# Performance work log

Hardware: AMD Instinct MI355X
Metric: run time of the kernel (lower is better)

Reference implementation:

```python
import jax, jax.numpy as jnp
import numpy as np

COS_BASIS_NO = 13
COS_SHIFT = 1.0
COS_SCALE = 3.0


def make_cos_basis(T_no):
    # [13, T_no] raised-cosine basis in log-time, matching the torch loop
    i = jnp.arange(COS_BASIS_NO, dtype=jnp.float32)[:, None]
    phi = 0.5 * jnp.pi * i
    x = jnp.arange(T_no, dtype=jnp.float32)[None, :]
    raw = COS_SCALE * jnp.log(x + COS_SHIFT)
    basis = 0.5 * jnp.cos(raw - phi) + 0.5
    mask = (raw >= phi - jnp.pi) & (raw <= phi + jnp.pi)
    return jnp.where(mask, basis, jnp.float32(0.0))


def causal_conv(x, kern):
    # x: [T, S], kern: [S, K] (unflipped, kern[:,0] = weight on x[t-1]).
    # Matches torch: pad K zeros in front, depthwise conv with flipped kernel, drop last.
    T, S = x.shape
    K = kern.shape[1]
    xp = jnp.pad(x, ((K, 0), (0, 0)))            # [T+K, S]
    lhs = xp.T[None]                              # [1, S, T+K]
    rhs = kern[:, None, ::-1]                     # [S, 1, K]
    out = jax.lax.conv_general_dilated(
        lhs, rhs, window_strides=(1,), padding='VALID',
        dimension_numbers=('NCW', 'OIW', 'NCW'), feature_group_count=S)
    return out[0].T[:-1]                          # [T, S]


def setup_inputs() -> dict:
    T_data, T_no, sub_no, E_no, I_no = 500000, 200, 20, 200, 50
    key = jax.random.key(0)
    ks = jax.random.split(key, 8)
    S_e = (jax.random.uniform(ks[0], (T_data, E_no)) < 0.05).astype(jnp.float32)
    S_i = (jax.random.uniform(ks[1], (T_data, I_no)) < 0.05).astype(jnp.float32)
    Z = (jax.random.uniform(ks[2], (T_data, sub_no)) < 0.10).astype(jnp.float32)
    C_syn_e = jax.nn.one_hot(jax.random.randint(ks[3], (E_no,), 0, sub_no), sub_no).T.astype(jnp.float32)
    C_syn_i = jax.nn.one_hot(jax.random.randint(ks[4], (I_no,), 0, sub_no), sub_no).T.astype(jnp.float32)
    C_den = (jax.random.uniform(ks[5], (sub_no, sub_no)) < 0.1).astype(jnp.float32)
    Tau_syn = jnp.ones((sub_no, 2), jnp.float32)
    Delta_syn = jnp.zeros((sub_no, 2), jnp.float32)
    W_syn = jnp.full((sub_no, 2), 0.01, jnp.float32)
    W_spk = jax.random.normal(ks[6], (sub_no, COS_BASIS_NO), jnp.float32) * 0.01
    W_hist = jax.random.normal(ks[7], (sub_no, COS_BASIS_NO), jnp.float32) * 0.1
    Theta = jnp.full((sub_no,), -5.0, jnp.float32)
    return dict(S_e=S_e, S_i=S_i, Z=Z, C_den=C_den, C_syn_e=C_syn_e, C_syn_i=C_syn_i,
                Tau_syn=Tau_syn, Delta_syn=Delta_syn, W_syn=W_syn, W_spk=W_spk,
                W_hist=W_hist, Theta=Theta, T_no=T_no)


def reference(S_e, S_i, Z, C_den, C_syn_e, C_syn_i, Tau_syn, Delta_syn, W_syn, W_spk, W_hist, Theta, T_no):
    # --- spike_convolve ---
    syn_e = S_e @ C_syn_e.T                       # [T, sub_no]
    syn_i = S_i @ C_syn_i.T
    t = jnp.arange(T_no, dtype=jnp.float32)[None, :]
    t_e = jnp.maximum(t - Delta_syn[:, 0:1], 0.0)
    t_i = jnp.maximum(t - Delta_syn[:, 1:2], 0.0)
    t_tau_e = t_e / Tau_syn[:, 0:1] ** 2
    t_tau_i = t_i / Tau_syn[:, 1:2] ** 2
    e_kern = t_tau_e * jnp.exp(-t_tau_e) * W_syn[:, 0:1] ** 2   # [sub_no, T_no]
    i_kern = -(t_tau_i * jnp.exp(-t_tau_i) * W_syn[:, 1:2] ** 2)
    syn = causal_conv(syn_e, e_kern) + causal_conv(syn_i, i_kern)
    # --- train_forward ---
    cos_basis = make_cos_basis(T_no)              # [13, T_no]
    spk_kern = W_spk @ cos_basis                  # [sub_no, T_no]
    hist_kern = W_hist @ cos_basis
    spk_filt = causal_conv(Z, spk_kern) @ C_den.T
    hist_filt = causal_conv(Z, hist_kern)
    P = jax.nn.sigmoid(syn + Theta[None, :] + hist_filt + spk_filt)
    out_filters = jnp.vstack((e_kern, i_kern, spk_kern, hist_kern))  # [4*sub_no, T_no]
    return P, out_filters
```

## Files before the change

### kernel.cpp

```cpp
#include <hip/hip_runtime.h>
#include <hip/hip_bf16.h>
#include <math.h>

typedef unsigned int u32;
typedef unsigned short u16;
typedef __bf16 bf16x8 __attribute__((ext_vector_type(8)));
typedef float f32x4 __attribute__((ext_vector_type(4)));
typedef u32 u32x4 __attribute__((ext_vector_type(4)));
typedef u32 u32x2 __attribute__((ext_vector_type(2)));

#define T_DATA 500000
#define KNO    200
#define SUB    20
#define E_NO   200
#define I_NO   50
#define NBAS   13
#define PI_F   3.14159265358979f
#define KKN    7
#define P_SZ   (T_DATA*SUB)
#define TCH    256
#define NCHUNKS_TOT ((T_DATA + TCH - 1)/TCH)
#define NST    29
#define WSTR   472

__device__ __forceinline__ float bf2f(u16 v){
  union { u32 u; float f; } x; x.u = ((u32)v) << 16; return x.f;
}
__device__ __forceinline__ u16 f2bf(float f){
  union { float f; u32 u; } x; x.f = f;
  u32 u = x.u;
  return (u16)((u + 0x7FFFu + ((u >> 16) & 1u)) >> 16);
}
__device__ __forceinline__ u16 trunc_bf(float f){
  union { float f; u32 u; } x; x.f = f;
  return (u16)(x.u >> 16);
}
__device__ __forceinline__ u32 f2u(float f){
  union { float f; u32 u; } x; x.f = f; return x.u;
}

__device__ __forceinline__ float filt_val(int type, int s, int j,
    const float* Tau, const float* Del, const float* Wsyn,
    const float* Wspk, const float* Whist){
  if (type < 2){
    float tau = Tau[s*2+type];
    float del = Del[s*2+type];
    float w   = Wsyn[s*2+type];
    float t   = fmaxf((float)j - del, 0.0f);
    float tt  = t / (tau*tau);
    float v   = tt * expf(-tt) * (w*w);
    return (type == 1) ? -v : v;
  } else {
    const float* W = (type == 2) ? Wspk : Whist;
    float raw = 3.0f * logf((float)j + 1.0f);
    float acc = 0.0f;
#pragma unroll
    for (int b = 0; b < NBAS; b++){
      float d = raw - 0.5f*PI_F*(float)b;
      float bas = (d >= -PI_F && d <= PI_F) ? (0.5f*cosf(d) + 0.5f) : 0.0f;
      acc += W[s*NBAS + b] * bas;
    }
    return acc;
  }
}

__global__ void k_setup(const float* Tau, const float* Del, const float* Wsyn,
                        const float* Wspk, const float* Whist,
                        const float* Ce, const float* Ci,
                        float* out, u16* afrag, u16* bfrag){
  int bid = blockIdx.x;
  int tid = threadIdx.x;
  if (bid < 80){
    int r = bid, type = r / SUB, s = r % SUB;
    for (int j = tid; j < KNO; j += 64)
      out[P_SZ + r*KNO + j] = filt_val(type, s, j, Tau, Del, Wsyn, Wspk, Whist);
  } else if (bid < 80 + 4*SUB*KKN){
    int b = bid - 80;
    int kk = b % KKN;
    int ts = b / KKN;
    int type = ts / SUB, s = ts % SUB;
    __shared__ float kf[KNO];
    for (int j = tid; j < KNO; j += 64)
      kf[j] = filt_val(type, s, j, Tau, Del, Wsyn, Wspk, Whist);
    __syncthreads();
    int l = tid;
    int m = l & 15, kg = l >> 4;
    int off = 200 - 32*kk;
    u32 p[4];
#pragma unroll
    for (int h = 0; h < 4; h++){
      int u0 = kg*8 + 2*h;
      int i0 = off + m - 1 - u0;
      int i1 = i0 - 1;
      u16 lo = (i0 >= 0 && i0 < KNO) ? f2bf(kf[i0]) : (u16)0;
      u16 hi = (i1 >= 0 && i1 < KNO) ? f2bf(kf[i1]) : (u16)0;
      p[h] = (u32)lo | ((u32)hi << 16);
    }
    u32* dst = (u32*)(afrag + (size_t)b*512 + l*8);
    dst[0]=p[0]; dst[1]=p[1]; dst[2]=p[2]; dst[3]=p[3];
  } else {
    const int NE = 2*7*512, NI = 2*2*512, NZ = 2*1*512;
    int b = bid - (80 + 4*SUB*KKN);
    for (int x = b*64 + tid; x < NE+NI+NZ; x += 40*64){
      int src, base, KT;
      if (x < NE){ src=0; base=x;       KT=7; }
      else if (x < NE+NI){ src=1; base=x-NE;    KT=2; }
      else {               src=2; base=x-NE-NI; KT=1; }
      int nt = base / (KT*512);
      int rem = base % (KT*512);
      int kt = rem / 512;
      int le = rem % 512;
      int l = le / 8, e = le % 8;
      int n = nt*16 + (l & 15);
      int k = kt*32 + (l >> 4)*8 + e;
      u16 v = 0;
      if (src == 0){ if (n < SUB && k < E_NO) v = trunc_bf(Ce[n*E_NO + k]); }
      else if (src == 1){ if (n < SUB && k < I_NO) v = trunc_bf(Ci[n*I_NO + k]); }
      else { if (n < SUB && k == n) v = trunc_bf(1.0f); }
      bfrag[x] = v;
    }
  }
}

template<int W, int KT>
__device__ __forceinline__ void stage1(const float* __restrict__ src,
                                       const u16* __restrict__ bfr,
                                       u16* __restrict__ wrow,
                                       long tw0, int wv, int lane){
  int m = lane & 15, kg = lane >> 4;
  const size_t NW = (size_t)T_DATA * W;
  for (int s = wv; s < NST; s += 8){
    long tr = tw0 + s*16 + m;
    u32 wb[KT][8];
#pragma unroll
    for (int kt = 0; kt < KT; kt++){
      bool skip;
      if (W == 200)      skip = (kt == 6) && (kg > 0);
      else if (W == 50)  skip = (kt == 1) && (kg == 3);
      else               skip = (kg == 3);
      if (skip || tr < 0 || tr >= T_DATA){
#pragma unroll
        for (int e = 0; e < 8; e++) wb[kt][e] = 0u;
      } else {
        size_t cs = (size_t)tr*W + kt*32 + kg*8;
        if (cs + 8 <= NW){
          if (W == 50){
            *(u32x2*)&wb[kt][0] = *(const u32x2*)(src + cs);
            *(u32x2*)&wb[kt][2] = *(const u32x2*)(src + cs + 2);
            *(u32x2*)&wb[kt][4] = *(const u32x2*)(src + cs + 4);
            *(u32x2*)&wb[kt][6] = *(const u32x2*)(src + cs + 6);
          } else {
            *(u32x4*)&wb[kt][0] = *(const u32x4*)(src + cs);
            *(u32x4*)&wb[kt][4] = *(const u32x4*)(src + cs + 4);
          }
        } else {
#pragma unroll
          for (int e = 0; e < 8; e++){
            size_t idx = cs + e;
            wb[kt][e] = (idx < NW) ? f2u(src[idx]) : 0u;
          }
        }
      }
    }
    f32x4 acc0 = {0.f,0.f,0.f,0.f}, acc1 = {0.f,0.f,0.f,0.f};
#pragma unroll
    for (int kt = 0; kt < KT; kt++){
      union { bf16x8 v; u16 h[8]; } au;
#pragma unroll
      for (int e = 0; e < 8; e++) au.h[e] = (u16)(wb[kt][e] >> 16);
      bf16x8 b0 = *(const bf16x8*)(bfr + kt*512 + lane*8);
      bf16x8 b1 = *(const bf16x8*)(bfr + (KT + kt)*512 + lane*8);
      acc0 = __builtin_amdgcn_mfma_f32_16x16x32_bf16(au.v, b0, acc0, 0, 0, 0);
      acc1 = __builtin_amdgcn_mfma_f32_16x16x32_bf16(au.v, b1, acc1, 0, 0, 0);
    }
    int i0 = s*16 + kg*4;
    {
      u32* d = (u32*)(wrow + (size_t)m*WSTR + i0);
      d[0] = (u32)f2bf(acc0[0]) | ((u32)f2bf(acc0[1]) << 16);
      d[1] = (u32)f2bf(acc0[2]) | ((u32)f2bf(acc0[3]) << 16);
    }
    if (m < SUB - 16){
      u32* d = (u32*)(wrow + (size_t)(16 + m)*WSTR + i0);
      d[0] = (u32)f2bf(acc1[0]) | ((u32)f2bf(acc1[1]) << 16);
      d[1] = (u32)f2bf(acc1[2]) | ((u32)f2bf(acc1[3]) << 16);
    }
  }
}

__global__ __launch_bounds__(512, 4) void k_mega(
    const float* __restrict__ S_e, const float* __restrict__ S_i,
    const float* __restrict__ Z, const u16* __restrict__ afrag,
    const u16* __restrict__ bfrag, const float* __restrict__ Cden,
    const float* __restrict__ Theta, float* __restrict__ out)
{
  __shared__ __align__(16) u16 win[3*SUB*WSTR];
  __shared__ float lcden[SUB*SUB];
  __shared__ float lth[SUB];

  int tid = threadIdx.x;
  for (int i = tid; i < SUB*SUB; i += 512) lcden[i] = Cden[i];
  if (tid < SUB) lth[tid] = Theta[tid];

  int bid = blockIdx.x;
  int xcd = bid & 7, sb = bid >> 3;
  const int q8 = NCHUNKS_TOT >> 3, r8 = NCHUNKS_TOT & 7;
  int c = (xcd < r8 ? xcd*(q8+1) : r8*(q8+1) + (xcd-r8)*q8) + sb;

  int wv = tid >> 6, lane = tid & 63;
  int m = lane & 15, kg = lane >> 4;
  long tw0 = (long)c*TCH - 200;

  stage1<200,7>(S_e, bfrag,                     win,                tw0, wv, lane);
  stage1<50, 2>(S_i, bfrag + 2*7*512,           win + SUB*WSTR,     tw0, wv, lane);
  stage1<20, 1>(Z,   bfrag + 2*7*512 + 2*2*512, win + 2*SUB*WSTR,   tw0, wv, lane);
  __syncthreads();

  int boffB = 16*m + 8*kg;
  int toff  = 16*m + 4*kg;
  f32x4 A0[5], A1[5];
  if (wv < 4){
    int ch0 = wv*5;
#pragma unroll
    for (int q = 0; q < 5; q++){
      int ch = ch0 + q;
      const u16* be = win + (size_t)(0*SUB + ch)*WSTR + boffB;
      const u16* bi = win + (size_t)(1*SUB + ch)*WSTR + boffB;
      const u16* ae = afrag + (size_t)((0*SUB + ch)*KKN)*512 + lane*8;
      const u16* ai = afrag + (size_t)((1*SUB + ch)*KKN)*512 + lane*8;
      f32x4 a = {0.f,0.f,0.f,0.f};
#pragma unroll
      for (int kk = 0; kk < KKN; kk++){
        a = __builtin_amdgcn_mfma_f32_16x16x32_bf16(
              *(const bf16x8*)(ae + kk*512), *(const bf16x8*)(be + 32*kk), a, 0,0,0);
        a = __builtin_amdgcn_mfma_f32_16x16x32_bf16(
              *(const bf16x8*)(ai + kk*512), *(const bf16x8*)(bi + 32*kk), a, 0,0,0);
      }
      A0[q] = a;
    }
  } else {
    int ch0 = (wv - 4)*5;
#pragma unroll
    for (int q = 0; q < 5; q++){
      int ch = ch0 + q;
      const u16* bz = win + (size_t)(2*SUB + ch)*WSTR + boffB;
      const u16* a2 = afrag + (size_t)((2*SUB + ch)*KKN)*512 + lane*8;
      const u16* a3 = afrag + (size_t)((3*SUB + ch)*KKN)*512 + lane*8;
      f32x4 s = {0.f,0.f,0.f,0.f}, h = {0.f,0.f,0.f,0.f};
#pragma unroll
      for (int kk = 0; kk < KKN; kk++){
        bf16x8 b = *(const bf16x8*)(bz + 32*kk);
        s = __builtin_amdgcn_mfma_f32_16x16x32_bf16(*(const bf16x8*)(a2 + kk*512), b, s, 0,0,0);
        h = __builtin_amdgcn_mfma_f32_16x16x32_bf16(*(const bf16x8*)(a3 + kk*512), b, h, 0,0,0);
      }
      A0[q] = s; A1[q] = h;
    }
  }
  __syncthreads();

  u16* rr = win;
  if (wv < 4){
#pragma unroll
    for (int q = 0; q < 5; q++){
      int ch = wv*5 + q;
      u32* d = (u32*)(rr + ch*TCH + toff);
      d[0] = (u32)f2bf(A0[q][0]) | ((u32)f2bf(A0[q][1]) << 16);
      d[1] = (u32)f2bf(A0[q][2]) | ((u32)f2bf(A0[q][3]) << 16);
    }
  } else {
#pragma unroll
    for (int q = 0; q < 5; q++){
      int ch = (wv - 4)*5 + q;
      u32* d1 = (u32*)(rr + (SUB + ch)*TCH + toff);
      d1[0] = (u32)f2bf(A0[q][0]) | ((u32)f2bf(A0[q][1]) << 16);
      d1[1] = (u32)f2bf(A0[q][2]) | ((u32)f2bf(A0[q][3]) << 16);
      u32* d2 = (u32*)(rr + (2*SUB + ch)*TCH + toff);
      d2[0] = (u32)f2bf(A1[q][0]) | ((u32)f2bf(A1[q][1]) << 16);
      d2[1] = (u32)f2bf(A1[q][2]) | ((u32)f2bf(A1[q][3]) << 16);
    }
  }
  __syncthreads();

  float* pbuf = (float*)win;
  int t = tid >> 1, h = tid & 1;
  float spkv[SUB];
#pragma unroll
  for (int s = 0; s < SUB; s++) spkv[s] = bf2f(rr[(SUB + s)*TCH + t]);
  float res[10];
#pragma unroll
  for (int j = 0; j < 10; j++){
    int sp = h*10 + j;
    float msum = bf2f(rr[sp*TCH + t]) + lth[sp] + bf2f(rr[(2*SUB + sp)*TCH + t]);
#pragma unroll
    for (int s = 0; s < SUB; s++) msum += lcden[sp*SUB + s] * spkv[s];
    res[j] = 1.0f/(1.0f + expf(-msum));
  }
  __syncthreads();
#pragma unroll
  for (int j = 0; j < 10; j++) pbuf[t*21 + h*10 + j] = res[j];
  __syncthreads();

  int t0c = c*TCH;
  int tv = min(TCH, T_DATA - t0c);
  int np4 = tv*SUB/4;
  for (int i = tid; i < np4; i += 512){
    int p = i*4;
    int tt = p/20, sp = p - tt*20;
    float4 v;
    v.x = pbuf[tt*21 + sp];   v.y = pbuf[tt*21 + sp+1];
    v.z = pbuf[tt*21 + sp+2]; v.w = pbuf[tt*21 + sp+3];
    *(float4*)(out + (size_t)t0c*SUB + p) = v;
  }
}

extern "C" void kernel_launch(void* const* d_in, const int* in_sizes, int n_in,
                              void* d_out, int out_size, void* d_ws, size_t ws_size,
                              hipStream_t stream){
  const float* S_e  = (const float*)d_in[0];
  const float* S_i  = (const float*)d_in[1];
  const float* Z    = (const float*)d_in[2];
  const float* Cden = (const float*)d_in[3];
  const float* C_e  = (const float*)d_in[4];
  const float* C_i  = (const float*)d_in[5];
  const float* Tau  = (const float*)d_in[6];
  const float* Del  = (const float*)d_in[7];
  const float* Wsyn = (const float*)d_in[8];
  const float* Wspk = (const float*)d_in[9];
  const float* Whist= (const float*)d_in[10];
  const float* Theta= (const float*)d_in[11];
  float* out = (float*)d_out;

  u16* afrag = (u16*)d_ws;
  u16* bfrag = afrag + (size_t)4*SUB*KKN*512;
  size_t need = ((size_t)4*SUB*KKN*512 + 10240) * 2;
  if (ws_size < need) return;

  k_setup<<<80 + 4*SUB*KKN + 40, 64, 0, stream>>>(
      Tau, Del, Wsyn, Wspk, Whist, C_e, C_i, out, afrag, bfrag);

  k_mega<<<NCHUNKS_TOT, 512, 0, stream>>>(
      S_e, S_i, Z, afrag, bfrag, Cden, Theta, out);
}
```

Baseline: 225.8 us.

## Software-pipeline stage-1 strip loads with MFMA across all three inputs

Splits the stage-1 routine into a load step and a matmul step, then interleaves the three input streams (S_e, S_i, Z). Each wave prefetches the next strip's global loads into registers while running MFMAs on the current strip. The aim is to hide global-memory latency behind compute and to keep more loads in flight per wave. The cost is higher register pressure from double-buffering about 80 u32 values per lane, which could lower occupancy under the 512x4 launch bounds.

```diff
diff --git a/kernel.cpp b/kernel.cpp
--- a/kernel.cpp
+++ b/kernel.cpp
@@ -123,67 +123,69 @@
 }
 
 template<int W, int KT>
-__device__ __forceinline__ void stage1(const float* __restrict__ src,
-                                       const u16* __restrict__ bfr,
-                                       u16* __restrict__ wrow,
-                                       long tw0, int wv, int lane){
-  int m = lane & 15, kg = lane >> 4;
+__device__ __forceinline__ void ld_strip(const float* __restrict__ src,
+                                         long tw0, int s, int m, int kg,
+                                         u32 (&wb)[KT][8]){
+  long tr = tw0 + (long)s*16 + m;
   const size_t NW = (size_t)T_DATA * W;
-  for (int s = wv; s < NST; s += 8){
-    long tr = tw0 + s*16 + m;
-    u32 wb[KT][8];
-#pragma unroll
-    for (int kt = 0; kt < KT; kt++){
-      bool skip;
-      if (W == 200)      skip = (kt == 6) && (kg > 0);
-      else if (W == 50)  skip = (kt == 1) && (kg == 3);
-      else               skip = (kg == 3);
-      if (skip || tr < 0 || tr >= T_DATA){
-#pragma unroll
-        for (int e = 0; e < 8; e++) wb[kt][e] = 0u;
+#pragma unroll
+  for (int kt = 0; kt < KT; kt++){
+    bool skip;
+    if (W == 200)      skip = (kt == 6) && (kg > 0);
+    else if (W == 50)  skip = (kt == 1) && (kg == 3);
+    else               skip = (kg == 3);
+    if (skip || tr < 0 || tr >= T_DATA){
+#pragma unroll
+      for (int e = 0; e < 8; e++) wb[kt][e] = 0u;
+    } else {
+      size_t cs = (size_t)tr*W + kt*32 + kg*8;
+      if (cs + 8 <= NW){
+        if (W == 50){
+          *(u32x2*)&wb[kt][0] = *(const u32x2*)(src + cs);
+          *(u32x2*)&wb[kt][2] = *(const u32x2*)(src + cs + 2);
+          *(u32x2*)&wb[kt][4] = *(const u32x2*)(src + cs + 4);
+          *(u32x2*)&wb[kt][6] = *(const u32x2*)(src + cs + 6);
+        } else {
+          *(u32x4*)&wb[kt][0] = *(const u32x4*)(src + cs);
+          *(u32x4*)&wb[kt][4] = *(const u32x4*)(src + cs + 4);
+        }
       } else {
-        size_t cs = (size_t)tr*W + kt*32 + kg*8;
-        if (cs + 8 <= NW){
-          if (W == 50){
-            *(u32x2*)&wb[kt][0] = *(const u32x2*)(src + cs);
-            *(u32x2*)&wb[kt][2] = *(const u32x2*)(src + cs + 2);
-            *(u32x2*)&wb[kt][4] = *(const u32x2*)(src + cs + 4);
-            *(u32x2*)&wb[kt][6] = *(const u32x2*)(src + cs + 6);
-          } else {
-            *(u32x4*)&wb[kt][0] = *(const u32x4*)(src + cs);
-            *(u32x4*)&wb[kt][4] = *(const u32x4*)(src + cs + 4);
-          }
-        } else {
-#pragma unroll
-          for (int e = 0; e < 8; e++){
-            size_t idx = cs + e;
-            wb[kt][e] = (idx < NW) ? f2u(src[idx]) : 0u;
-          }
+#pragma unroll
+        for (int e = 0; e < 8; e++){
+          size_t idx = cs + e;
+          wb[kt][e] = (idx < NW) ? f2u(src[idx]) : 0u;
         }
       }
     }
-    f32x4 acc0 = {0.f,0.f,0.f,0.f}, acc1 = {0.f,0.f,0.f,0.f};
-#pragma unroll
-    for (int kt = 0; kt < KT; kt++){
-      union { bf16x8 v; u16 h[8]; } au;
-#pragma unroll
-      for (int e = 0; e < 8; e++) au.h[e] = (u16)(wb[kt][e] >> 16);
-      bf16x8 b0 = *(const bf16x8*)(bfr + kt*512 + lane*8);
-      bf16x8 b1 = *(const bf16x8*)(bfr + (KT + kt)*512 + lane*8);
-      acc0 = __builtin_amdgcn_mfma_f32_16x16x32_bf16(au.v, b0, acc0, 0, 0, 0);
-      acc1 = __builtin_amdgcn_mfma_f32_16x16x32_bf16(au.v, b1, acc1, 0, 0, 0);
-    }
-    int i0 = s*16 + kg*4;
-    {
-      u32* d = (u32*)(wrow + (size_t)m*WSTR + i0);
-      d[0] = (u32)f2bf(acc0[0]) | ((u32)f2bf(acc0[1]) << 16);
-      d[1] = (u32)f2bf(acc0[2]) | ((u32)f2bf(acc0[3]) << 16);
-    }
-    if (m < SUB - 16){
-      u32* d = (u32*)(wrow + (size_t)(16 + m)*WSTR + i0);
-      d[0] = (u32)f2bf(acc1[0]) | ((u32)f2bf(acc1[1]) << 16);
-      d[1] = (u32)f2bf(acc1[2]) | ((u32)f2bf(acc1[3]) << 16);
-    }
+  }
+}
+
+template<int W, int KT>
+__device__ __forceinline__ void mm_strip(const u16* __restrict__ bfr,
+                                         const u32 (&wb)[KT][8],
+                                         u16* __restrict__ wrow,
+                                         int s, int m, int kg, int lane){
+  f32x4 acc0 = {0.f,0.f,0.f,0.f}, acc1 = {0.f,0.f,0.f,0.f};
+#pragma unroll
+  for (int kt = 0; kt < KT; kt++){
+    union { bf16x8 v; u16 h[8]; } au;
+#pragma unroll
+    for (int e = 0; e < 8; e++) au.h[e] = (u16)(wb[kt][e] >> 16);
+    bf16x8 b0 = *(const bf16x8*)(bfr + kt*512 + lane*8);
+    bf16x8 b1 = *(const bf16x8*)(bfr + (KT + kt)*512 + lane*8);
+    acc0 = __builtin_amdgcn_mfma_f32_16x16x32_bf16(au.v, b0, acc0, 0, 0, 0);
+    acc1 = __builtin_amdgcn_mfma_f32_16x16x32_bf16(au.v, b1, acc1, 0, 0, 0);
+  }
+  int i0 = s*16 + kg*4;
+  {
+    u32* d = (u32*)(wrow + (size_t)m*WSTR + i0);
+    d[0] = (u32)f2bf(acc0[0]) | ((u32)f2bf(acc0[1]) << 16);
+    d[1] = (u32)f2bf(acc0[2]) | ((u32)f2bf(acc0[3]) << 16);
+  }
+  if (m < SUB - 16){
+    u32* d = (u32*)(wrow + (size_t)(16 + m)*WSTR + i0);
+    d[0] = (u32)f2bf(acc1[0]) | ((u32)f2bf(acc1[1]) << 16);
+    d[1] = (u32)f2bf(acc1[2]) | ((u32)f2bf(acc1[3]) << 16);
   }
 }
 
@@ -210,9 +212,33 @@
   int m = lane & 15, kg = lane >> 4;
   long tw0 = (long)c*TCH - 200;
 
-  stage1<200,7>(S_e, bfrag,                     win,                tw0, wv, lane);
-  stage1<50, 2>(S_i, bfrag + 2*7*512,           win + SUB*WSTR,     tw0, wv, lane);
-  stage1<20, 1>(Z,   bfrag + 2*7*512 + 2*2*512, win + 2*SUB*WSTR,   tw0, wv, lane);
+  {
+    const u16* bfE = bfrag;
+    const u16* bfI = bfrag + 2*7*512;
+    const u16* bfZ = bfrag + 2*7*512 + 2*2*512;
+    u16* wE = win;
+    u16* wI = win + SUB*WSTR;
+    u16* wZ = win + 2*SUB*WSTR;
+    u32 wbE[KKN][8];
+    u32 wbI[2][8];
+    u32 wbZ[1][8];
+    ld_strip<200,7>(S_e, tw0, wv, m, kg, wbE);
+    ld_strip<50, 2>(S_i, tw0, wv, m, kg, wbI);
+    ld_strip<20, 1>(Z,   tw0, wv, m, kg, wbZ);
+#pragma unroll
+    for (int r = 0; r < 4; r++){
+      int sc = wv + r*8;
+      int sn = sc + 8;
+      if (sc < NST){
+        mm_strip<200,7>(bfE, wbE, wE, sc, m, kg, lane);
+        if (sn < NST) ld_strip<200,7>(S_e, tw0, sn, m, kg, wbE);
+        mm_strip<50, 2>(bfI, wbI, wI, sc, m, kg, lane);
+        if (sn < NST) ld_strip<50, 2>(S_i, tw0, sn, m, kg, wbI);
+        mm_strip<20, 1>(bfZ, wbZ, wZ, sc, m, kg, lane);
+        if (sn < NST) ld_strip<20, 1>(Z,   tw0, sn, m, kg, wbZ);
+      }
+    }
+  }
   __syncthreads();
 
   int boffB = 16*m + 8*kg;
```

After: 385.2 us. 1.71x slower.

## Split fused kernel into a gather/projection pass and a windowed convolution pass

Applied to the files above, without the earlier changes.

The fused kernel recomputed the input projections for each 256-step chunk plus a 200-step halo, so every block reread overlapping rows of S_e, S_i and Z. This change moves the projection into its own kernel, which computes each 16-row tile once and writes channel-major bf16 intermediates to the workspace. The convolution kernel then loads its windows from those intermediates. This removes the redundant halo reads and projection work, and costs an extra launch plus a write and reread of about 60 MB of bf16 intermediates.

```diff
diff --git a/kernel.cpp b/kernel.cpp
--- a/kernel.cpp
+++ b/kernel.cpp
@@ -18,9 +18,10 @@
 #define PI_F   3.14159265358979f
 #define KKN    7
 #define P_SZ   (T_DATA*SUB)
+#define MT_TOT (T_DATA/16)
 #define TCH    256
 #define NCHUNKS_TOT ((T_DATA + TCH - 1)/TCH)
-#define NST    29
+#define GBLK   ((MT_TOT + 3)/4)
 #define WSTR   472
 
 __device__ __forceinline__ float bf2f(u16 v){
@@ -123,75 +124,87 @@
 }
 
 template<int W, int KT>
-__device__ __forceinline__ void stage1(const float* __restrict__ src,
-                                       const u16* __restrict__ bfr,
-                                       u16* __restrict__ wrow,
-                                       long tw0, int wv, int lane){
+__device__ __forceinline__ void gather_body(int bid, const float* __restrict__ src,
+                                            const u16* __restrict__ bfrag,
+                                            u16* __restrict__ dst){
+  int wv = threadIdx.x >> 6, lane = threadIdx.x & 63;
+  int mt = bid*4 + wv;
+  if (mt >= MT_TOT) return;
+  int t0 = mt*16;
   int m = lane & 15, kg = lane >> 4;
   const size_t NW = (size_t)T_DATA * W;
-  for (int s = wv; s < NST; s += 8){
-    long tr = tw0 + s*16 + m;
-    u32 wb[KT][8];
-#pragma unroll
-    for (int kt = 0; kt < KT; kt++){
-      bool skip;
-      if (W == 200)      skip = (kt == 6) && (kg > 0);
-      else if (W == 50)  skip = (kt == 1) && (kg == 3);
-      else               skip = (kg == 3);
-      if (skip || tr < 0 || tr >= T_DATA){
-#pragma unroll
-        for (int e = 0; e < 8; e++) wb[kt][e] = 0u;
+
+  u32 wb[KT][8];
+#pragma unroll
+  for (int kt = 0; kt < KT; kt++){
+    bool skip;
+    if (W == 200)      skip = (kt == 6) && (kg > 0);
+    else if (W == 50)  skip = (kt == 1) && (kg == 3);
+    else               skip = (kg == 3);
+    size_t cs = (size_t)(t0 + m)*W + kt*32 + kg*8;
+    if (skip){
+#pragma unroll
+      for (int e = 0; e < 8; e++) wb[kt][e] = 0u;
+    } else if (cs + 8 <= NW){
+      if (W == 50){
+        *(u32x2*)&wb[kt][0] = *(const u32x2*)(src + cs);
+        *(u32x2*)&wb[kt][2] = *(const u32x2*)(src + cs + 2);
+        *(u32x2*)&wb[kt][4] = *(const u32x2*)(src + cs + 4);
+        *(u32x2*)&wb[kt][6] = *(const u32x2*)(src + cs + 6);
       } else {
-        size_t cs = (size_t)tr*W + kt*32 + kg*8;
-        if (cs + 8 <= NW){
-          if (W == 50){
-            *(u32x2*)&wb[kt][0] = *(const u32x2*)(src + cs);
-            *(u32x2*)&wb[kt][2] = *(const u32x2*)(src + cs + 2);
-            *(u32x2*)&wb[kt][4] = *(const u32x2*)(src + cs + 4);
-            *(u32x2*)&wb[kt][6] = *(const u32x2*)(src + cs + 6);
-          } else {
-            *(u32x4*)&wb[kt][0] = *(const u32x4*)(src + cs);
-            *(u32x4*)&wb[kt][4] = *(const u32x4*)(src + cs + 4);
-          }
-        } else {
-#pragma unroll
-          for (int e = 0; e < 8; e++){
-            size_t idx = cs + e;
-            wb[kt][e] = (idx < NW) ? f2u(src[idx]) : 0u;
-          }
-        }
-      }
-    }
-    f32x4 acc0 = {0.f,0.f,0.f,0.f}, acc1 = {0.f,0.f,0.f,0.f};
-#pragma unroll
-    for (int kt = 0; kt < KT; kt++){
-      union { bf16x8 v; u16 h[8]; } au;
-#pragma unroll
-      for (int e = 0; e < 8; e++) au.h[e] = (u16)(wb[kt][e] >> 16);
-      bf16x8 b0 = *(const bf16x8*)(bfr + kt*512 + lane*8);
-      bf16x8 b1 = *(const bf16x8*)(bfr + (KT + kt)*512 + lane*8);
-      acc0 = __builtin_amdgcn_mfma_f32_16x16x32_bf16(au.v, b0, acc0, 0, 0, 0);
-      acc1 = __builtin_amdgcn_mfma_f32_16x16x32_bf16(au.v, b1, acc1, 0, 0, 0);
-    }
-    int i0 = s*16 + kg*4;
-    {
-      u32* d = (u32*)(wrow + (size_t)m*WSTR + i0);
-      d[0] = (u32)f2bf(acc0[0]) | ((u32)f2bf(acc0[1]) << 16);
-      d[1] = (u32)f2bf(acc0[2]) | ((u32)f2bf(acc0[3]) << 16);
-    }
-    if (m < SUB - 16){
-      u32* d = (u32*)(wrow + (size_t)(16 + m)*WSTR + i0);
-      d[0] = (u32)f2bf(acc1[0]) | ((u32)f2bf(acc1[1]) << 16);
-      d[1] = (u32)f2bf(acc1[2]) | ((u32)f2bf(acc1[3]) << 16);
-    }
-  }
-}
-
-__global__ __launch_bounds__(512, 4) void k_mega(
+        *(u32x4*)&wb[kt][0] = *(const u32x4*)(src + cs);
+        *(u32x4*)&wb[kt][4] = *(const u32x4*)(src + cs + 4);
+      }
+    } else {
+#pragma unroll
+      for (int e = 0; e < 8; e++){
+        size_t idx = cs + e;
+        wb[kt][e] = (idx < NW) ? f2u(src[idx]) : 0u;
+      }
+    }
+  }
+
+  f32x4 acc0 = {0.f,0.f,0.f,0.f}, acc1 = {0.f,0.f,0.f,0.f};
+#pragma unroll
+  for (int kt = 0; kt < KT; kt++){
+    union { bf16x8 v; u16 h[8]; } au;
+#pragma unroll
+    for (int e = 0; e < 8; e++) au.h[e] = (u16)(wb[kt][e] >> 16);
+    bf16x8 b0 = *(const bf16x8*)(bfrag + kt*512 + lane*8);
+    bf16x8 b1 = *(const bf16x8*)(bfrag + (KT + kt)*512 + lane*8);
+    acc0 = __builtin_amdgcn_mfma_f32_16x16x32_bf16(au.v, b0, acc0, 0, 0, 0);
+    acc1 = __builtin_amdgcn_mfma_f32_16x16x32_bf16(au.v, b1, acc1, 0, 0, 0);
+  }
+  int i0 = kg*4;
+  {
+    u32 lo = (u32)f2bf(acc0[0]) | ((u32)f2bf(acc0[1]) << 16);
+    u32 hi = (u32)f2bf(acc0[2]) | ((u32)f2bf(acc0[3]) << 16);
+    u32* d = (u32*)(dst + (size_t)m*T_DATA + t0 + i0);
+    d[0] = lo; d[1] = hi;
+  }
+  if (m < SUB - 16){
+    u32 lo = (u32)f2bf(acc1[0]) | ((u32)f2bf(acc1[1]) << 16);
+    u32 hi = (u32)f2bf(acc1[2]) | ((u32)f2bf(acc1[3]) << 16);
+    u32* d = (u32*)(dst + (size_t)(16 + m)*T_DATA + t0 + i0);
+    d[0] = lo; d[1] = hi;
+  }
+}
+
+__global__ __launch_bounds__(256, 4) void k_gather_all(
     const float* __restrict__ S_e, const float* __restrict__ S_i,
-    const float* __restrict__ Z, const u16* __restrict__ afrag,
-    const u16* __restrict__ bfrag, const float* __restrict__ Cden,
-    const float* __restrict__ Theta, float* __restrict__ out)
+    const float* __restrict__ Z, const u16* __restrict__ bfrag,
+    u16* __restrict__ xe, u16* __restrict__ xi, u16* __restrict__ zt){
+  int bid = blockIdx.x;
+  if (bid < GBLK)            gather_body<200,7>(bid,          S_e, bfrag,                       xe);
+  else if (bid < 2*GBLK)     gather_body<50, 2>(bid - GBLK,   S_i, bfrag + 2*7*512,             xi);
+  else                       gather_body<20, 1>(bid - 2*GBLK, Z,   bfrag + 2*7*512 + 2*2*512,   zt);
+}
+
+__global__ __launch_bounds__(512, 2) void k_conv2(
+    const u16* __restrict__ xe, const u16* __restrict__ xi,
+    const u16* __restrict__ zt, const u16* __restrict__ afrag,
+    const float* __restrict__ Cden, const float* __restrict__ Theta,
+    float* __restrict__ out)
 {
   __shared__ __align__(16) u16 win[3*SUB*WSTR];
   __shared__ float lcden[SUB*SUB];
@@ -208,11 +221,26 @@
 
   int wv = tid >> 6, lane = tid & 63;
   int m = lane & 15, kg = lane >> 4;
-  long tw0 = (long)c*TCH - 200;
-
-  stage1<200,7>(S_e, bfrag,                     win,                tw0, wv, lane);
-  stage1<50, 2>(S_i, bfrag + 2*7*512,           win + SUB*WSTR,     tw0, wv, lane);
-  stage1<20, 1>(Z,   bfrag + 2*7*512 + 2*2*512, win + 2*SUB*WSTR,   tw0, wv, lane);
+  long t0w = (long)c*TCH - 200;
+
+  for (int i = tid; i < 3*SUB*58; i += 512){
+    int arr = i / (SUB*58);
+    int rem = i - arr*(SUB*58);
+    int ch  = rem / 58;
+    int i8  = rem - ch*58;
+    long g0 = t0w + i8*8;
+    const u16* gp = (arr == 0 ? xe : (arr == 1 ? xi : zt)) + (size_t)ch*T_DATA;
+    u16* lp = win + (size_t)(arr*SUB + ch)*WSTR + i8*8;
+    if (g0 >= 0 && g0 + 8 <= T_DATA){
+      *(bf16x8*)lp = *(const bf16x8*)(gp + g0);
+    } else {
+#pragma unroll
+      for (int e = 0; e < 8; e++){
+        long g = g0 + e;
+        lp[e] = (g >= 0 && g < T_DATA) ? gp[g] : (u16)0;
+      }
+    }
+  }
   __syncthreads();
 
   int boffB = 16*m + 8*kg;
@@ -329,14 +357,18 @@
   const float* Theta= (const float*)d_in[11];
   float* out = (float*)d_out;
 
-  u16* afrag = (u16*)d_ws;
+  u16* xe    = (u16*)d_ws;
+  u16* xi    = xe + (size_t)SUB*T_DATA;
+  u16* zt    = xi + (size_t)SUB*T_DATA;
+  u16* afrag = zt + (size_t)SUB*T_DATA;
   u16* bfrag = afrag + (size_t)4*SUB*KKN*512;
-  size_t need = ((size_t)4*SUB*KKN*512 + 10240) * 2;
+  size_t need = ((size_t)3*SUB*T_DATA + (size_t)4*SUB*KKN*512 + 10240) * 2;
   if (ws_size < need) return;
 
   k_setup<<<80 + 4*SUB*KKN + 40, 64, 0, stream>>>(
       Tau, Del, Wsyn, Wspk, Whist, C_e, C_i, out, afrag, bfrag);
 
-  k_mega<<<NCHUNKS_TOT, 512, 0, stream>>>(
-      S_e, S_i, Z, afrag, bfrag, Cden, Theta, out);
-}
+  k_gather_all<<<3*GBLK, 256, 0, stream>>>(S_e, S_i, Z, bfrag, xe, xi, zt);
+
+  k_conv2<<<NCHUNKS_TOT, 512, 0, stream>>>(xe, xi, zt, afrag, Cden, Theta, out);
+}
```

Measured after the change: 212.6 us. 5.8% less time.
